# Kernel optimization log

Hardware: AMD Instinct MI355X
Metric: run time of the kernel (lower is better)

## Reference

```python
import jax, jax.numpy as jnp
import numpy as np

BN_EPS = 1e-5

def _vq(x, embed):
    # x: (..., dim), embed: (dim, K). Nearest-codeword lookup with straight-through.
    dim = x.shape[-1]
    flat = x.reshape(-1, dim)
    dist = (flat * flat).sum(1, keepdims=True) - 2.0 * (flat @ embed) + (embed * embed).sum(0, keepdims=True)
    ids = jnp.argmin(dist, axis=1)
    q = jnp.take(embed.T, ids, axis=0).reshape(x.shape)
    diff = jnp.mean((jax.lax.stop_gradient(q) - x) ** 2)
    q = x + jax.lax.stop_gradient(q - x)
    return q, diff

def _weight_quantize(W, embed, in_mem, out_mem):
    # W: (out_f, in_f). Group W.T into (out_g, in_g, in_mem*out_mem) blocks,
    # VQ each block, scatter back to (out_f, in_f). Matches torch chunk/stack loops.
    out_f, in_f = W.shape
    in_g, out_g = in_f // in_mem, out_f // out_mem
    g = W.T.reshape(in_g, in_mem, out_g, out_mem).transpose(2, 0, 1, 3).reshape(out_g, in_g, in_mem * out_mem)
    q, diff = _vq(g, embed)
    qW = q.reshape(out_g, in_g, in_mem, out_mem).transpose(0, 3, 1, 2).reshape(out_f, in_f)
    return qW, diff

def _bn(x, gamma, beta):
    # training-mode BatchNorm1d: biased batch variance
    mu = x.mean(axis=0)
    var = ((x - mu) ** 2).mean(axis=0)
    return (x - mu) * jax.lax.rsqrt(var + BN_EPS) * gamma + beta


def setup_inputs() -> dict:
    key = jax.random.key(0)
    ks = jax.random.split(key, 8)
    B, D_IN, H, D_OUT, K = 65536, 784, 512, 10, 512
    s = 0.05
    return {
        "x": jax.random.normal(ks[0], (B, D_IN), jnp.float32),
        "W1": jax.random.normal(ks[1], (H, D_IN), jnp.float32) * s,
        "b1": jnp.zeros((H,), jnp.float32),
        "gamma1": jnp.ones((H,), jnp.float32),
        "beta1": jnp.zeros((H,), jnp.float32),
        "E1": jax.random.normal(ks[2], (28, K), jnp.float32) * s,  # dim = in_mem(7)*out_mem(4)
        "W2": jax.random.normal(ks[3], (H, H), jnp.float32) * s,
        "b2": jnp.zeros((H,), jnp.float32),
        "E2": jax.random.normal(ks[4], (16, K), jnp.float32) * s,  # dim = in_mem(16)*out_mem(1)
        "W3": jax.random.normal(ks[5], (D_OUT, H), jnp.float32) * s,
        "b3": jnp.zeros((D_OUT,), jnp.float32),
    }


def reference(x, W1, b1, gamma1, beta1, E1, W2, b2, E2, W3, b3):
    qW1, diff1 = _weight_quantize(W1, E1, 7, 4)
    h = jax.nn.relu(x @ qW1.T + b1)
    qW2, diff2 = _weight_quantize(W2, E2, 16, 1)
    h = jax.nn.relu(_bn(h, gamma1, beta1) @ qW2.T + b2)
    out = h @ W3.T + b3
    return out, diff1 + diff2
```

## Files before the change

### kernel.cpp

```cpp
#include <hip/hip_runtime.h>
#include <stdint.h>

#define BATCH   65536
#define D_IN    784
#define KP      800
#define HDIM    512
#define D_OUT   10
#define NCODE   512
#define HT_LD   136

typedef _Float16 f16;
typedef _Float16 f16x8 __attribute__((ext_vector_type(8)));
typedef float    f32x4 __attribute__((ext_vector_type(4)));

__device__ __forceinline__ void gld_lds16(const void* g, void* l) {
  __builtin_amdgcn_global_load_lds((const __attribute__((address_space(1))) void*)g,
                                   (__attribute__((address_space(3))) void*)l, 16, 0, 0);
}

__global__ void k_convert_x(const float* __restrict__ x, f16* __restrict__ xh) {
  int t = blockIdx.x * 256 + threadIdx.x;
  int r = t / 100;
  int c = (t - r * 100) * 8;
  f16x8 o;
  if (c < D_IN) {
    const float4 a = *(const float4*)(x + (size_t)r * D_IN + c);
    const float4 b = *(const float4*)(x + (size_t)r * D_IN + c + 4);
    o[0]=(f16)a.x; o[1]=(f16)a.y; o[2]=(f16)a.z; o[3]=(f16)a.w;
    o[4]=(f16)b.x; o[5]=(f16)b.y; o[6]=(f16)b.z; o[7]=(f16)b.w;
  } else {
    #pragma unroll
    for (int j = 0; j < 8; ++j) o[j] = (f16)0.f;
  }
  *(f16x8*)(xh + (size_t)r * KP + c) = o;
}

__global__ void k_vq1(const float* __restrict__ W1, const float* __restrict__ E1,
                      f16* __restrict__ qW1, float* __restrict__ diffacc) {
  #pragma clang fp contract(off)
  __shared__ float E1s[28 * NCODE];
  __shared__ float Ts[NCODE];
  for (int i = threadIdx.x; i < 28 * NCODE; i += 256) E1s[i] = E1[i];
  __syncthreads();
  for (int k = threadIdx.x; k < NCODE; k += 256) {
    float e0 = E1s[k];
    float t = e0 * e0;
    for (int j = 1; j < 28; ++j) {
      float e = E1s[j * NCODE + k];
      float ee = e * e;
      t = t + ee;
    }
    Ts[k] = t;
  }
  __syncthreads();
  const int wid = threadIdx.x >> 6, lane = threadIdx.x & 63;
  const int bid = blockIdx.x * 4 + wid;
  const int og = bid / 112, ig = bid % 112;
  float v[28], vv[28];
  #pragma unroll
  for (int j = 0; j < 28; ++j) {
    int om = j & 3, im = j >> 2;
    v[j] = W1[(og * 4 + om) * D_IN + ig * 7 + im];
    vv[j] = v[j] * v[j];
  }
  float r[8];
  #pragma unroll
  for (int j = 0; j < 8; ++j) r[j] = vv[j];
  #pragma unroll
  for (int j = 0; j < 8; ++j) r[j] = r[j] + vv[8 + j];
  #pragma unroll
  for (int j = 0; j < 8; ++j) r[j] = r[j] + vv[16 + j];
  float s = ((r[0] + r[1]) + (r[2] + r[3])) + ((r[4] + r[5]) + (r[6] + r[7]));
  s = s + vv[24]; s = s + vv[25]; s = s + vv[26]; s = s + vv[27];

  float bestd = 1e30f; int bestk = 0x7fffffff;
  for (int t = 0; t < 8; ++t) {
    int k = t * 64 + lane;
    float dot = 0.f;
    #pragma unroll
    for (int j = 0; j < 28; ++j) dot = __builtin_fmaf(v[j], E1s[j * NCODE + k], dot);
    float d = (s - 2.0f * dot) + Ts[k];
    if (d < bestd || (d == bestd && k < bestk)) { bestd = d; bestk = k; }
  }
  for (int off = 32; off; off >>= 1) {
    float d2 = __shfl_down(bestd, off, 64);
    int   k2 = __shfl_down(bestk, off, 64);
    if (d2 < bestd || (d2 == bestd && k2 < bestk)) { bestd = d2; bestk = k2; }
  }
  int kstar = __shfl(bestk, 0, 64);
  float sq = 0.f;
  if (lane < 28) {
    int om = lane & 3, im = lane >> 2;
    float q = E1s[lane * NCODE + kstar];
    qW1[(size_t)(og * 4 + om) * KP + ig * 7 + im] = (f16)q;
    float dd = q - v[lane]; sq = dd * dd;
  }
  for (int off = 32; off; off >>= 1) sq += __shfl_down(sq, off, 64);
  if (lane == 0) atomicAdd(&diffacc[bid & 127], sq);
}

__global__ void k_vq2(const float* __restrict__ W2, const float* __restrict__ E2,
                      f16* __restrict__ qW2, float* __restrict__ diffacc) {
  #pragma clang fp contract(off)
  __shared__ float E2s[16 * NCODE];
  __shared__ float Ts[NCODE];
  for (int i = threadIdx.x; i < 16 * NCODE; i += 256) E2s[i] = E2[i];
  __syncthreads();
  for (int k = threadIdx.x; k < NCODE; k += 256) {
    float e0 = E2s[k];
    float t = e0 * e0;
    for (int j = 1; j < 16; ++j) {
      float e = E2s[j * NCODE + k];
      float ee = e * e;
      t = t + ee;
    }
    Ts[k] = t;
  }
  __syncthreads();
  const int wid = threadIdx.x >> 6, lane = threadIdx.x & 63;
  const int bid = blockIdx.x * 4 + wid;
  const int og = bid >> 5, ig = bid & 31;
  float v[16], vv[16];
  #pragma unroll
  for (int j = 0; j < 16; ++j) {
    v[j] = W2[og * HDIM + ig * 16 + j];
    vv[j] = v[j] * v[j];
  }
  float r[8];
  #pragma unroll
  for (int j = 0; j < 8; ++j) r[j] = vv[j];
  #pragma unroll
  for (int j = 0; j < 8; ++j) r[j] = r[j] + vv[8 + j];
  float s = ((r[0] + r[1]) + (r[2] + r[3])) + ((r[4] + r[5]) + (r[6] + r[7]));

  float bestd = 1e30f; int bestk = 0x7fffffff;
  for (int t = 0; t < 8; ++t) {
    int k = t * 64 + lane;
    float dot = 0.f;
    #pragma unroll
    for (int j = 0; j < 16; ++j) dot = __builtin_fmaf(v[j], E2s[j * NCODE + k], dot);
    float d = (s - 2.0f * dot) + Ts[k];
    if (d < bestd || (d == bestd && k < bestk)) { bestd = d; bestk = k; }
  }
  for (int off = 32; off; off >>= 1) {
    float d2 = __shfl_down(bestd, off, 64);
    int   k2 = __shfl_down(bestk, off, 64);
    if (d2 < bestd || (d2 == bestd && k2 < bestk)) { bestd = d2; bestk = k2; }
  }
  int kstar = __shfl(bestk, 0, 64);
  float sq = 0.f;
  if (lane < 16) {
    float q = E2s[lane * NCODE + kstar];
    qW2[(size_t)og * HDIM + ig * 16 + lane] = (f16)q;
    float dd = q - v[lane]; sq = dd * dd;
  }
  for (int off = 32; off; off >>= 1) sq += __shfl_down(sq, off, 64);
  if (lane == 0) atomicAdd(&diffacc[bid & 127], sq);
}

__global__ void k_gemm1(const f16* __restrict__ A, const f16* __restrict__ Bw,
                        const float* __restrict__ bias, f16* __restrict__ C,
                        float* __restrict__ statacc) {
  __shared__ __align__(16) char lds_all[HT_LD * 128 * 2];
  __shared__ float cls[128], cls2[128];
  f16* As = (f16*)lds_all;
  f16* Bs = (f16*)(lds_all + 8192);
  f16* ht = (f16*)lds_all;
  const int tid = threadIdx.x;
  const int bn = blockIdx.x & 3;
  const int bm = blockIdx.x >> 2;
  const int lane = tid & 63, wid = tid >> 6;
  const int waveM = wid & 1, waveN = wid >> 1;
  const int l15 = lane & 15, quad = lane >> 4;

  if (tid < 128) cls[tid] = 0.f; else cls2[tid - 128] = 0.f;

  const int c0 = tid, c1 = tid + 256;
  const f16* gA0 = A + (size_t)(bm * 128 + (c0 >> 2)) * KP + (c0 & 3) * 8;
  const f16* gA1 = A + (size_t)(bm * 128 + (c1 >> 2)) * KP + (c1 & 3) * 8;
  const f16* gB0 = Bw + (size_t)(bn * 128 + (c0 >> 2)) * KP + (c0 & 3) * 8;
  const f16* gB1 = Bw + (size_t)(bn * 128 + (c1 >> 2)) * KP + (c1 & 3) * 8;
  f16* lA0 = As + c0 * 8; f16* lA1 = As + c1 * 8;
  f16* lB0 = Bs + c0 * 8; f16* lB1 = Bs + c1 * 8;

  f32x4 acc[4][4];
  #pragma unroll
  for (int i = 0; i < 4; ++i)
    #pragma unroll
    for (int j = 0; j < 4; ++j) acc[i][j] = (f32x4){0.f, 0.f, 0.f, 0.f};

  const int aoff = (waveM * 64 + l15) * 32 + quad * 8;
  const int boff = (waveN * 64 + l15) * 32 + quad * 8;

  for (int k0 = 0; k0 < KP; k0 += 32) {
    gld_lds16(gA0 + k0, lA0);
    gld_lds16(gA1 + k0, lA1);
    gld_lds16(gB0 + k0, lB0);
    gld_lds16(gB1 + k0, lB1);
    __syncthreads();
    f16x8 af[4], bf[4];
    #pragma unroll
    for (int i = 0; i < 4; ++i) af[i] = *(const f16x8*)(As + aoff + i * 16 * 32);
    #pragma unroll
    for (int j = 0; j < 4; ++j) bf[j] = *(const f16x8*)(Bs + boff + j * 16 * 32);
    #pragma unroll
    for (int i = 0; i < 4; ++i)
      #pragma unroll
      for (int j = 0; j < 4; ++j)
        acc[i][j] = __builtin_amdgcn_mfma_f32_16x16x32_f16(af[i], bf[j], acc[i][j], 0, 0, 0);
    __syncthreads();
  }
  const int colbase = bn * 128 + waveN * 64 + l15;
  float bcol[4];
  #pragma unroll
  for (int j = 0; j < 4; ++j) bcol[j] = bias[colbase + j * 16];
  float cs[4] = {0.f,0.f,0.f,0.f}, cs2[4] = {0.f,0.f,0.f,0.f};
  #pragma unroll
  for (int i = 0; i < 4; ++i)
    #pragma unroll
    for (int r2 = 0; r2 < 4; ++r2) {
      int rloc = waveM * 64 + quad * 4 + i * 16 + r2;
      #pragma unroll
      for (int j = 0; j < 4; ++j) {
        float v = acc[i][j][r2] + bcol[j];
        v = v > 0.f ? v : 0.f;
        ht[rloc * HT_LD + waveN * 64 + j * 16 + l15] = (f16)v;
        cs[j] += v; cs2[j] += v * v;
      }
    }
  #pragma unroll
  for (int j = 0; j < 4; ++j) {
    cs[j]  += __shfl_xor(cs[j], 16, 64);  cs[j]  += __shfl_xor(cs[j], 32, 64);
    cs2[j] += __shfl_xor(cs2[j], 16, 64); cs2[j] += __shfl_xor(cs2[j], 32, 64);
  }
  if (quad == 0) {
    #pragma unroll
    for (int j = 0; j < 4; ++j) {
      atomicAdd(&cls[waveN * 64 + j * 16 + l15], cs[j]);
      atomicAdd(&cls2[waveN * 64 + j * 16 + l15], cs2[j]);
    }
  }
  __syncthreads();
  if (tid < 128) atomicAdd(&statacc[256 + bn * 128 + tid], cls[tid]);
  else           atomicAdd(&statacc[768 + bn * 128 + (tid - 128)], cls2[tid - 128]);
  {
    const int rloc = tid >> 1, half = tid & 1;
    f16* crow = C + (size_t)(bm * 128 + rloc) * HDIM + bn * 128 + half * 64;
    const f16* srow = ht + rloc * HT_LD + half * 64;
    #pragma unroll
    for (int j = 0; j < 8; ++j)
      *(f16x8*)(crow + j * 8) = *(const f16x8*)(srow + j * 8);
  }
}

__global__ void k_bnprep(const float* __restrict__ acc, const float* __restrict__ gamma,
                         const float* __restrict__ beta, float* __restrict__ ab,
                         const float* __restrict__ W3, f16* __restrict__ W3h,
                         float* __restrict__ diff_out) {
  const int c = threadIdx.x;
  const float inv = 1.f / 65536.f;
  float mu = acc[256 + c] * inv;
  float msq = acc[768 + c] * inv;
  float var = msq - mu * mu;
  float a = gamma[c] / sqrtf(var + 1e-5f);
  ab[c] = a;
  ab[512 + c] = beta[c] - mu * a;
  #pragma unroll
  for (int o = 0; o < 16; ++o)
    W3h[o * HDIM + c] = (o < D_OUT) ? (f16)W3[o * HDIM + c] : (f16)0.f;
  if (c == 0) {
    float s1 = 0.f, s2 = 0.f;
    for (int i = 0; i < 128; ++i) { s1 += acc[i]; s2 += acc[128 + i]; }
    diff_out[0] = s1 * (1.f / 401408.f) + s2 * (1.f / 262144.f);
  }
}

__global__ void k_bnfold(f16* __restrict__ qW2, const float* __restrict__ ab,
                         const float* __restrict__ b2, float* __restrict__ bias2) {
  __shared__ float red[256];
  const int n = blockIdx.x, t = threadIdx.x;
  float partial = 0.f;
  #pragma unroll
  for (int kk = 0; kk < 2; ++kk) {
    int k = t + kk * 256;
    float w = (float)qW2[n * HDIM + k];
    partial += ab[512 + k] * w;
    qW2[n * HDIM + k] = (f16)(ab[k] * w);
  }
  red[t] = partial; __syncthreads();
  for (int s = 128; s > 0; s >>= 1) { if (t < s) red[t] += red[t + s]; __syncthreads(); }
  if (t == 0) bias2[n] = b2[n] + red[0];
}

__global__ void k_gemm2f(const f16* __restrict__ A, const f16* __restrict__ Bw,
                         const float* __restrict__ bias2, const f16* __restrict__ W3h,
                         const float* __restrict__ b3, float* __restrict__ out) {
  __shared__ __align__(16) char lds_all[HT_LD * 128 * 2];
  f16* As = (f16*)lds_all;
  f16* Bs = (f16*)(lds_all + 8192);
  f16* ht = (f16*)lds_all;
  const int tid = threadIdx.x;
  const int bn = blockIdx.x & 3;
  const int bm = blockIdx.x >> 2;
  const int lane = tid & 63, wid = tid >> 6;
  const int waveM = wid & 1, waveN = wid >> 1;
  const int l15 = lane & 15, quad = lane >> 4;

  const int c0 = tid, c1 = tid + 256;
  const f16* gA0 = A + (size_t)(bm * 128 + (c0 >> 2)) * HDIM + (c0 & 3) * 8;
  const f16* gA1 = A + (size_t)(bm * 128 + (c1 >> 2)) * HDIM + (c1 & 3) * 8;
  const f16* gB0 = Bw + (size_t)(bn * 128 + (c0 >> 2)) * HDIM + (c0 & 3) * 8;
  const f16* gB1 = Bw + (size_t)(bn * 128 + (c1 >> 2)) * HDIM + (c1 & 3) * 8;
  f16* lA0 = As + c0 * 8; f16* lA1 = As + c1 * 8;
  f16* lB0 = Bs + c0 * 8; f16* lB1 = Bs + c1 * 8;

  f32x4 acc[4][4];
  #pragma unroll
  for (int i = 0; i < 4; ++i)
    #pragma unroll
    for (int j = 0; j < 4; ++j) acc[i][j] = (f32x4){0.f, 0.f, 0.f, 0.f};

  const int aoff = (waveM * 64 + l15) * 32 + quad * 8;
  const int boff = (waveN * 64 + l15) * 32 + quad * 8;

  for (int k0 = 0; k0 < HDIM; k0 += 32) {
    gld_lds16(gA0 + k0, lA0);
    gld_lds16(gA1 + k0, lA1);
    gld_lds16(gB0 + k0, lB0);
    gld_lds16(gB1 + k0, lB1);
    __syncthreads();
    f16x8 af[4], bf[4];
    #pragma unroll
    for (int i = 0; i < 4; ++i) af[i] = *(const f16x8*)(As + aoff + i * 16 * 32);
    #pragma unroll
    for (int j = 0; j < 4; ++j) bf[j] = *(const f16x8*)(Bs + boff + j * 16 * 32);
    #pragma unroll
    for (int i = 0; i < 4; ++i)
      #pragma unroll
      for (int j = 0; j < 4; ++j)
        acc[i][j] = __builtin_amdgcn_mfma_f32_16x16x32_f16(af[i], bf[j], acc[i][j], 0, 0, 0);
    __syncthreads();
  }
  const int colbase = bn * 128 + waveN * 64 + l15;
  float bcol[4];
  #pragma unroll
  for (int j = 0; j < 4; ++j) bcol[j] = bias2[colbase + j * 16];
  #pragma unroll
  for (int i = 0; i < 4; ++i)
    #pragma unroll
    for (int r2 = 0; r2 < 4; ++r2) {
      int rloc = waveM * 64 + quad * 4 + i * 16 + r2;
      #pragma unroll
      for (int j = 0; j < 4; ++j) {
        float v = acc[i][j][r2] + bcol[j];
        v = v > 0.f ? v : 0.f;
        ht[rloc * HT_LD + waveN * 64 + j * 16 + l15] = (f16)v;
      }
    }
  __syncthreads();
  f32x4 oacc[2];
  oacc[0] = (f32x4){0.f,0.f,0.f,0.f}; oacc[1] = (f32x4){0.f,0.f,0.f,0.f};
  #pragma unroll
  for (int ks = 0; ks < 4; ++ks) {
    f16x8 bfr = *(const f16x8*)(W3h + l15 * HDIM + bn * 128 + ks * 32 + quad * 8);
    #pragma unroll
    for (int i2 = 0; i2 < 2; ++i2) {
      f16x8 afr = *(const f16x8*)(ht + (wid * 32 + i2 * 16 + l15) * HT_LD + ks * 32 + quad * 8);
      oacc[i2] = __builtin_amdgcn_mfma_f32_16x16x32_f16(afr, bfr, oacc[i2], 0, 0, 0);
    }
  }
  if (l15 < D_OUT) {
    float badd = (bn == 0) ? b3[l15] : 0.f;
    #pragma unroll
    for (int i2 = 0; i2 < 2; ++i2)
      #pragma unroll
      for (int r2 = 0; r2 < 4; ++r2) {
        int row = bm * 128 + wid * 32 + i2 * 16 + quad * 4 + r2;
        atomicAdd(&out[(size_t)row * D_OUT + l15], oacc[i2][r2] + badd);
      }
  }
}

extern "C" void kernel_launch(void* const* d_in, const int* in_sizes, int n_in,
                              void* d_out, int out_size, void* d_ws, size_t ws_size,
                              hipStream_t stream) {
  const float* x     = (const float*)d_in[0];
  const float* W1    = (const float*)d_in[1];
  const float* b1    = (const float*)d_in[2];
  const float* gamma = (const float*)d_in[3];
  const float* beta  = (const float*)d_in[4];
  const float* E1    = (const float*)d_in[5];
  const float* W2    = (const float*)d_in[6];
  const float* b2    = (const float*)d_in[7];
  const float* E2    = (const float*)d_in[8];
  const float* W3    = (const float*)d_in[9];
  const float* b3    = (const float*)d_in[10];
  float* out = (float*)d_out;

  char* ws = (char*)d_ws;
  float* accum = (float*)ws;
  f16* qW1h = (f16*)(ws + 8192);
  f16* qW2h = (f16*)(ws + 827392);
  f16* W3h  = (f16*)(ws + 1351680);
  float* ab = (float*)(ws + 1368064);
  float* bias2 = (float*)(ws + 1372160);
  f16* xh   = (f16*)(ws + 1376256);
  f16* h    = (f16*)(ws + 106233856);

  hipMemsetAsync(ws, 0, 827392, stream);
  hipMemsetAsync(d_out, 0, (size_t)out_size * 4, stream);
  k_convert_x<<<25600, 256, 0, stream>>>(x, xh);
  k_vq1<<<3584, 256, 0, stream>>>(W1, E1, qW1h, accum);
  k_vq2<<<4096, 256, 0, stream>>>(W2, E2, qW2h, accum + 128);
  k_gemm1<<<2048, 256, 0, stream>>>(xh, qW1h, b1, h, accum);
  k_bnprep<<<1, 512, 0, stream>>>(accum, gamma, beta, ab, W3, W3h, out + (size_t)BATCH * D_OUT);
  k_bnfold<<<512, 256, 0, stream>>>(qW2h, ab, b2, bias2);
  k_gemm2f<<<2048, 256, 0, stream>>>(h, qW2h, bias2, W3h, b3, out);
}
```

Before: 600.5 us.

## Fuse fp32-to-fp16 input conversion into GEMM1 and deepen K tile to 64

```diff
diff --git a/kernel.cpp b/kernel.cpp
--- a/kernel.cpp
+++ b/kernel.cpp
@@ -3,7 +3,7 @@
 
 #define BATCH   65536
 #define D_IN    784
-#define KP      800
+#define KP      832
 #define HDIM    512
 #define D_OUT   10
 #define NCODE   512
@@ -16,23 +16,6 @@
 __device__ __forceinline__ void gld_lds16(const void* g, void* l) {
   __builtin_amdgcn_global_load_lds((const __attribute__((address_space(1))) void*)g,
                                    (__attribute__((address_space(3))) void*)l, 16, 0, 0);
-}
-
-__global__ void k_convert_x(const float* __restrict__ x, f16* __restrict__ xh) {
-  int t = blockIdx.x * 256 + threadIdx.x;
-  int r = t / 100;
-  int c = (t - r * 100) * 8;
-  f16x8 o;
-  if (c < D_IN) {
-    const float4 a = *(const float4*)(x + (size_t)r * D_IN + c);
-    const float4 b = *(const float4*)(x + (size_t)r * D_IN + c + 4);
-    o[0]=(f16)a.x; o[1]=(f16)a.y; o[2]=(f16)a.z; o[3]=(f16)a.w;
-    o[4]=(f16)b.x; o[5]=(f16)b.y; o[6]=(f16)b.z; o[7]=(f16)b.w;
-  } else {
-    #pragma unroll
-    for (int j = 0; j < 8; ++j) o[j] = (f16)0.f;
-  }
-  *(f16x8*)(xh + (size_t)r * KP + c) = o;
 }
 
 __global__ void k_vq1(const float* __restrict__ W1, const float* __restrict__ E1,
@@ -158,30 +141,41 @@
   if (lane == 0) atomicAdd(&diffacc[bid & 127], sq);
 }
 
-__global__ void k_gemm1(const f16* __restrict__ A, const f16* __restrict__ Bw,
-                        const float* __restrict__ bias, f16* __restrict__ C,
-                        float* __restrict__ statacc) {
+__global__ void __launch_bounds__(256, 4)
+k_gemm1(const float* __restrict__ X, const f16* __restrict__ Bw,
+        const float* __restrict__ bias, f16* __restrict__ C,
+        float* __restrict__ statacc) {
   __shared__ __align__(16) char lds_all[HT_LD * 128 * 2];
   __shared__ float cls[128], cls2[128];
   f16* As = (f16*)lds_all;
-  f16* Bs = (f16*)(lds_all + 8192);
+  f16* Bs = (f16*)(lds_all + 16384);
   f16* ht = (f16*)lds_all;
   const int tid = threadIdx.x;
-  const int bn = blockIdx.x & 3;
-  const int bm = blockIdx.x >> 2;
+  const int logical = ((blockIdx.x & 7) << 8) + (blockIdx.x >> 3);
+  const int bn = logical & 3;
+  const int bm = logical >> 2;
   const int lane = tid & 63, wid = tid >> 6;
   const int waveM = wid & 1, waveN = wid >> 1;
   const int l15 = lane & 15, quad = lane >> 4;
 
   if (tid < 128) cls[tid] = 0.f; else cls2[tid - 128] = 0.f;
 
-  const int c0 = tid, c1 = tid + 256;
-  const f16* gA0 = A + (size_t)(bm * 128 + (c0 >> 2)) * KP + (c0 & 3) * 8;
-  const f16* gA1 = A + (size_t)(bm * 128 + (c1 >> 2)) * KP + (c1 & 3) * 8;
-  const f16* gB0 = Bw + (size_t)(bn * 128 + (c0 >> 2)) * KP + (c0 & 3) * 8;
-  const f16* gB1 = Bw + (size_t)(bn * 128 + (c1 >> 2)) * KP + (c1 & 3) * 8;
-  f16* lA0 = As + c0 * 8; f16* lA1 = As + c1 * 8;
-  f16* lB0 = Bs + c0 * 8; f16* lB1 = Bs + c1 * 8;
+  const f16* gB[4]; f16* lB[4];
+  #pragma unroll
+  for (int s = 0; s < 4; ++s) {
+    int slot = tid + s * 256;
+    int ks = slot >> 9, r2 = (slot >> 2) & 127, c = slot & 3;
+    gB[s] = Bw + (size_t)(bn * 128 + r2) * KP + ks * 32 + c * 8;
+    lB[s] = Bs + slot * 8;
+  }
+  const int cA = tid & 3;
+  const float* gA[4]; f16* lA[4];
+  #pragma unroll
+  for (int s = 0; s < 4; ++s) {
+    int r2 = (tid >> 2) + (s & 1) * 64;
+    gA[s] = X + (size_t)(bm * 128 + r2) * D_IN + (s >> 1) * 32 + cA * 8;
+    lA[s] = As + (tid + s * 256) * 8;
+  }
 
   f32x4 acc[4][4];
   #pragma unroll
@@ -192,22 +186,43 @@
   const int aoff = (waveM * 64 + l15) * 32 + quad * 8;
   const int boff = (waveN * 64 + l15) * 32 + quad * 8;
 
-  for (int k0 = 0; k0 < KP; k0 += 32) {
-    gld_lds16(gA0 + k0, lA0);
-    gld_lds16(gA1 + k0, lA1);
-    gld_lds16(gB0 + k0, lB0);
-    gld_lds16(gB1 + k0, lB1);
+  for (int k0 = 0; k0 < KP; k0 += 64) {
+    #pragma unroll
+    for (int s = 0; s < 4; ++s) gld_lds16(gB[s] + k0, lB[s]);
+    float4 ra[8];
+    #pragma unroll
+    for (int s = 0; s < 4; ++s) {
+      int gcol = k0 + (s >> 1) * 32 + cA * 8;
+      ra[2 * s]     = (float4){0.f, 0.f, 0.f, 0.f};
+      ra[2 * s + 1] = (float4){0.f, 0.f, 0.f, 0.f};
+      if (gcol < D_IN) {
+        ra[2 * s]     = *(const float4*)(gA[s] + k0);
+        ra[2 * s + 1] = *(const float4*)(gA[s] + k0 + 4);
+      }
+    }
+    #pragma unroll
+    for (int s = 0; s < 4; ++s) {
+      f16x8 o;
+      o[0] = (f16)ra[2 * s].x;     o[1] = (f16)ra[2 * s].y;
+      o[2] = (f16)ra[2 * s].z;     o[3] = (f16)ra[2 * s].w;
+      o[4] = (f16)ra[2 * s + 1].x; o[5] = (f16)ra[2 * s + 1].y;
+      o[6] = (f16)ra[2 * s + 1].z; o[7] = (f16)ra[2 * s + 1].w;
+      *(f16x8*)lA[s] = o;
+    }
     __syncthreads();
-    f16x8 af[4], bf[4];
-    #pragma unroll
-    for (int i = 0; i < 4; ++i) af[i] = *(const f16x8*)(As + aoff + i * 16 * 32);
-    #pragma unroll
-    for (int j = 0; j < 4; ++j) bf[j] = *(const f16x8*)(Bs + boff + j * 16 * 32);
-    #pragma unroll
-    for (int i = 0; i < 4; ++i)
-      #pragma unroll
-      for (int j = 0; j < 4; ++j)
-        acc[i][j] = __builtin_amdgcn_mfma_f32_16x16x32_f16(af[i], bf[j], acc[i][j], 0, 0, 0);
+    #pragma unroll
+    for (int ks = 0; ks < 2; ++ks) {
+      f16x8 af[4], bf[4];
+      #pragma unroll
+      for (int i = 0; i < 4; ++i) af[i] = *(const f16x8*)(As + ks * 4096 + aoff + i * 512);
+      #pragma unroll
+      for (int j = 0; j < 4; ++j) bf[j] = *(const f16x8*)(Bs + ks * 4096 + boff + j * 512);
+      #pragma unroll
+      for (int i = 0; i < 4; ++i)
+        #pragma unroll
+        for (int j = 0; j < 4; ++j)
+          acc[i][j] = __builtin_amdgcn_mfma_f32_16x16x32_f16(af[i], bf[j], acc[i][j], 0, 0, 0);
+    }
     __syncthreads();
   }
   const int colbase = bn * 128 + waveN * 64 + l15;
@@ -292,27 +307,32 @@
   if (t == 0) bias2[n] = b2[n] + red[0];
 }
 
-__global__ void k_gemm2f(const f16* __restrict__ A, const f16* __restrict__ Bw,
-                         const float* __restrict__ bias2, const f16* __restrict__ W3h,
-                         const float* __restrict__ b3, float* __restrict__ out) {
+__global__ void __launch_bounds__(256, 4)
+k_gemm2f(const f16* __restrict__ A, const f16* __restrict__ Bw,
+         const float* __restrict__ bias2, const f16* __restrict__ W3h,
+         const float* __restrict__ b3, float* __restrict__ out) {
   __shared__ __align__(16) char lds_all[HT_LD * 128 * 2];
   f16* As = (f16*)lds_all;
-  f16* Bs = (f16*)(lds_all + 8192);
+  f16* Bs = (f16*)(lds_all + 16384);
   f16* ht = (f16*)lds_all;
   const int tid = threadIdx.x;
-  const int bn = blockIdx.x & 3;
-  const int bm = blockIdx.x >> 2;
+  const int logical = ((blockIdx.x & 7) << 8) + (blockIdx.x >> 3);
+  const int bn = logical & 3;
+  const int bm = logical >> 2;
   const int lane = tid & 63, wid = tid >> 6;
   const int waveM = wid & 1, waveN = wid >> 1;
   const int l15 = lane & 15, quad = lane >> 4;
 
-  const int c0 = tid, c1 = tid + 256;
-  const f16* gA0 = A + (size_t)(bm * 128 + (c0 >> 2)) * HDIM + (c0 & 3) * 8;
-  const f16* gA1 = A + (size_t)(bm * 128 + (c1 >> 2)) * HDIM + (c1 & 3) * 8;
-  const f16* gB0 = Bw + (size_t)(bn * 128 + (c0 >> 2)) * HDIM + (c0 & 3) * 8;
-  const f16* gB1 = Bw + (size_t)(bn * 128 + (c1 >> 2)) * HDIM + (c1 & 3) * 8;
-  f16* lA0 = As + c0 * 8; f16* lA1 = As + c1 * 8;
-  f16* lB0 = Bs + c0 * 8; f16* lB1 = Bs + c1 * 8;
+  const f16* gA[4]; const f16* gB[4]; f16* lA[4]; f16* lB[4];
+  #pragma unroll
+  for (int s = 0; s < 4; ++s) {
+    int slot = tid + s * 256;
+    int ks = slot >> 9, r2 = (slot >> 2) & 127, c = slot & 3;
+    gA[s] = A  + (size_t)(bm * 128 + r2) * HDIM + ks * 32 + c * 8;
+    gB[s] = Bw + (size_t)(bn * 128 + r2) * HDIM + ks * 32 + c * 8;
+    lA[s] = As + slot * 8;
+    lB[s] = Bs + slot * 8;
+  }
 
   f32x4 acc[4][4];
   #pragma unroll
@@ -323,22 +343,26 @@
   const int aoff = (waveM * 64 + l15) * 32 + quad * 8;
   const int boff = (waveN * 64 + l15) * 32 + quad * 8;
 
-  for (int k0 = 0; k0 < HDIM; k0 += 32) {
-    gld_lds16(gA0 + k0, lA0);
-    gld_lds16(gA1 + k0, lA1);
-    gld_lds16(gB0 + k0, lB0);
-    gld_lds16(gB1 + k0, lB1);
+  for (int k0 = 0; k0 < HDIM; k0 += 64) {
+    #pragma unroll
+    for (int s = 0; s < 4; ++s) {
+      gld_lds16(gA[s] + k0, lA[s]);
+      gld_lds16(gB[s] + k0, lB[s]);
+    }
     __syncthreads();
-    f16x8 af[4], bf[4];
-    #pragma unroll
-    for (int i = 0; i < 4; ++i) af[i] = *(const f16x8*)(As + aoff + i * 16 * 32);
-    #pragma unroll
-    for (int j = 0; j < 4; ++j) bf[j] = *(const f16x8*)(Bs + boff + j * 16 * 32);
-    #pragma unroll
-    for (int i = 0; i < 4; ++i)
-      #pragma unroll
-      for (int j = 0; j < 4; ++j)
-        acc[i][j] = __builtin_amdgcn_mfma_f32_16x16x32_f16(af[i], bf[j], acc[i][j], 0, 0, 0);
+    #pragma unroll
+    for (int ks = 0; ks < 2; ++ks) {
+      f16x8 af[4], bf[4];
+      #pragma unroll
+      for (int i = 0; i < 4; ++i) af[i] = *(const f16x8*)(As + ks * 4096 + aoff + i * 512);
+      #pragma unroll
+      for (int j = 0; j < 4; ++j) bf[j] = *(const f16x8*)(Bs + ks * 4096 + boff + j * 512);
+      #pragma unroll
+      for (int i = 0; i < 4; ++i)
+        #pragma unroll
+        for (int j = 0; j < 4; ++j)
+          acc[i][j] = __builtin_amdgcn_mfma_f32_16x16x32_f16(af[i], bf[j], acc[i][j], 0, 0, 0);
+    }
     __syncthreads();
   }
   const int colbase = bn * 128 + waveN * 64 + l15;
@@ -400,19 +424,17 @@
   char* ws = (char*)d_ws;
   float* accum = (float*)ws;
   f16* qW1h = (f16*)(ws + 8192);
-  f16* qW2h = (f16*)(ws + 827392);
-  f16* W3h  = (f16*)(ws + 1351680);
-  float* ab = (float*)(ws + 1368064);
-  float* bias2 = (float*)(ws + 1372160);
-  f16* xh   = (f16*)(ws + 1376256);
-  f16* h    = (f16*)(ws + 106233856);
-
-  hipMemsetAsync(ws, 0, 827392, stream);
+  f16* qW2h = (f16*)(ws + 860160);
+  f16* W3h  = (f16*)(ws + 1384448);
+  float* ab = (float*)(ws + 1400832);
+  float* bias2 = (float*)(ws + 1404928);
+  f16* h    = (f16*)(ws + 1409024);
+
+  hipMemsetAsync(ws, 0, 860160, stream);
   hipMemsetAsync(d_out, 0, (size_t)out_size * 4, stream);
-  k_convert_x<<<25600, 256, 0, stream>>>(x, xh);
   k_vq1<<<3584, 256, 0, stream>>>(W1, E1, qW1h, accum);
   k_vq2<<<4096, 256, 0, stream>>>(W2, E2, qW2h, accum + 128);
-  k_gemm1<<<2048, 256, 0, stream>>>(xh, qW1h, b1, h, accum);
+  k_gemm1<<<2048, 256, 0, stream>>>(x, qW1h, b1, h, accum);
   k_bnprep<<<1, 512, 0, stream>>>(accum, gamma, beta, ab, W3, W3h, out + (size_t)BATCH * D_OUT);
   k_bnfold<<<512, 256, 0, stream>>>(qW2h, ab, b2, bias2);
   k_gemm2f<<<2048, 256, 0, stream>>>(h, qW2h, bias2, W3h, b3, out);
```

After: 564.1 us. -6.1%, faster.

## Fuse fp32-to-fp16 x conversion into GEMM1 and double-buffer both GEMM main loops

Applied to the files above, without the earlier changes.

```diff
diff --git a/kernel.cpp b/kernel.cpp
--- a/kernel.cpp
+++ b/kernel.cpp
@@ -18,22 +18,8 @@
                                    (__attribute__((address_space(3))) void*)l, 16, 0, 0);
 }
 
-__global__ void k_convert_x(const float* __restrict__ x, f16* __restrict__ xh) {
-  int t = blockIdx.x * 256 + threadIdx.x;
-  int r = t / 100;
-  int c = (t - r * 100) * 8;
-  f16x8 o;
-  if (c < D_IN) {
-    const float4 a = *(const float4*)(x + (size_t)r * D_IN + c);
-    const float4 b = *(const float4*)(x + (size_t)r * D_IN + c + 4);
-    o[0]=(f16)a.x; o[1]=(f16)a.y; o[2]=(f16)a.z; o[3]=(f16)a.w;
-    o[4]=(f16)b.x; o[5]=(f16)b.y; o[6]=(f16)b.z; o[7]=(f16)b.w;
-  } else {
-    #pragma unroll
-    for (int j = 0; j < 8; ++j) o[j] = (f16)0.f;
-  }
-  *(f16x8*)(xh + (size_t)r * KP + c) = o;
-}
+#define MEMFENCE asm volatile("" ::: "memory")
+#define BARRIER() do { MEMFENCE; __builtin_amdgcn_s_barrier(); MEMFENCE; } while (0)
 
 __global__ void k_vq1(const float* __restrict__ W1, const float* __restrict__ E1,
                       f16* __restrict__ qW1, float* __restrict__ diffacc) {
@@ -158,30 +144,29 @@
   if (lane == 0) atomicAdd(&diffacc[bid & 127], sq);
 }
 
-__global__ void k_gemm1(const f16* __restrict__ A, const f16* __restrict__ Bw,
-                        const float* __restrict__ bias, f16* __restrict__ C,
-                        float* __restrict__ statacc) {
+__global__ void __launch_bounds__(256, 4)
+k_gemm1(const float* __restrict__ X, const f16* __restrict__ Bw,
+        const float* __restrict__ bias, f16* __restrict__ C,
+        float* __restrict__ statacc) {
   __shared__ __align__(16) char lds_all[HT_LD * 128 * 2];
   __shared__ float cls[128], cls2[128];
-  f16* As = (f16*)lds_all;
-  f16* Bs = (f16*)(lds_all + 8192);
   f16* ht = (f16*)lds_all;
   const int tid = threadIdx.x;
-  const int bn = blockIdx.x & 3;
-  const int bm = blockIdx.x >> 2;
+  const int logical = ((blockIdx.x & 7) << 8) + (blockIdx.x >> 3);
+  const int bn = logical & 3;
+  const int bm = logical >> 2;
   const int lane = tid & 63, wid = tid >> 6;
   const int waveM = wid & 1, waveN = wid >> 1;
   const int l15 = lane & 15, quad = lane >> 4;
 
   if (tid < 128) cls[tid] = 0.f; else cls2[tid - 128] = 0.f;
 
-  const int c0 = tid, c1 = tid + 256;
-  const f16* gA0 = A + (size_t)(bm * 128 + (c0 >> 2)) * KP + (c0 & 3) * 8;
-  const f16* gA1 = A + (size_t)(bm * 128 + (c1 >> 2)) * KP + (c1 & 3) * 8;
-  const f16* gB0 = Bw + (size_t)(bn * 128 + (c0 >> 2)) * KP + (c0 & 3) * 8;
-  const f16* gB1 = Bw + (size_t)(bn * 128 + (c1 >> 2)) * KP + (c1 & 3) * 8;
-  f16* lA0 = As + c0 * 8; f16* lA1 = As + c1 * 8;
-  f16* lB0 = Bs + c0 * 8; f16* lB1 = Bs + c1 * 8;
+  const int cA = tid & 3;
+  const int r0 = tid >> 2;
+  const float* gX0 = X + (size_t)(bm * 128 + r0) * D_IN;
+  const float* gX1 = gX0 + (size_t)64 * D_IN;
+  const f16*  gB0 = Bw + (size_t)(bn * 128 + r0) * KP + cA * 8;
+  const f16*  gB1 = gB0 + (size_t)64 * KP;
 
   f32x4 acc[4][4];
   #pragma unroll
@@ -192,23 +177,77 @@
   const int aoff = (waveM * 64 + l15) * 32 + quad * 8;
   const int boff = (waveN * 64 + l15) * 32 + quad * 8;
 
-  for (int k0 = 0; k0 < KP; k0 += 32) {
-    gld_lds16(gA0 + k0, lA0);
-    gld_lds16(gA1 + k0, lA1);
-    gld_lds16(gB0 + k0, lB0);
-    gld_lds16(gB1 + k0, lB1);
-    __syncthreads();
+  float4 ra0, ra1, ra2, ra3;
+  auto issueA = [&](int k0) {
+    int gc = k0 + cA * 8;
+    int gco = gc < D_IN ? gc : 0;
+    ra0 = *(const float4*)(gX0 + gco);
+    ra1 = *(const float4*)(gX0 + gco + 4);
+    ra2 = *(const float4*)(gX1 + gco);
+    ra3 = *(const float4*)(gX1 + gco + 4);
+  };
+  auto writeA = [&](int k0, f16* dstA) {
+    bool valid = (k0 + cA * 8) < D_IN;
+    float4 a0 = ra0, a1 = ra1, b0 = ra2, b1 = ra3;
+    if (!valid) {
+      a0 = (float4){0.f,0.f,0.f,0.f}; a1 = a0; b0 = a0; b1 = a0;
+    }
+    f16x8 o0, o1;
+    o0[0]=(f16)a0.x; o0[1]=(f16)a0.y; o0[2]=(f16)a0.z; o0[3]=(f16)a0.w;
+    o0[4]=(f16)a1.x; o0[5]=(f16)a1.y; o0[6]=(f16)a1.z; o0[7]=(f16)a1.w;
+    o1[0]=(f16)b0.x; o1[1]=(f16)b0.y; o1[2]=(f16)b0.z; o1[3]=(f16)b0.w;
+    o1[4]=(f16)b1.x; o1[5]=(f16)b1.y; o1[6]=(f16)b1.z; o1[7]=(f16)b1.w;
+    *(f16x8*)(dstA + tid * 8) = o0;
+    *(f16x8*)(dstA + tid * 8 + 2048) = o1;
+  };
+  auto issueB = [&](int k0, f16* dstB) {
+    gld_lds16(gB0 + k0, dstB + tid * 8);
+    gld_lds16(gB1 + k0, dstB + tid * 8 + 2048);
+  };
+  auto mma = [&](const f16* A_, const f16* B_) {
     f16x8 af[4], bf[4];
     #pragma unroll
-    for (int i = 0; i < 4; ++i) af[i] = *(const f16x8*)(As + aoff + i * 16 * 32);
-    #pragma unroll
-    for (int j = 0; j < 4; ++j) bf[j] = *(const f16x8*)(Bs + boff + j * 16 * 32);
+    for (int i = 0; i < 4; ++i) af[i] = *(const f16x8*)(A_ + aoff + i * 512);
+    #pragma unroll
+    for (int j = 0; j < 4; ++j) bf[j] = *(const f16x8*)(B_ + boff + j * 512);
     #pragma unroll
     for (int i = 0; i < 4; ++i)
       #pragma unroll
       for (int j = 0; j < 4; ++j)
         acc[i][j] = __builtin_amdgcn_mfma_f32_16x16x32_f16(af[i], bf[j], acc[i][j], 0, 0, 0);
-    __syncthreads();
+  };
+
+  const int NT = KP / 32;
+  issueA(0);
+  MEMFENCE;
+  issueB(0, (f16*)(lds_all + 16384));
+  MEMFENCE;
+  writeA(0, (f16*)lds_all);
+  issueA(32);
+  asm volatile("s_waitcnt vmcnt(4) lgkmcnt(0)" ::: "memory");
+  BARRIER();
+
+  for (int k = 0; k < NT; ++k) {
+    const int cur = k & 1;
+    f16* Asc = (f16*)(lds_all + cur * 8192);
+    f16* Bsc = (f16*)(lds_all + 16384 + cur * 8192);
+    f16* Asn = (f16*)(lds_all + (cur ^ 1) * 8192);
+    f16* Bsn = (f16*)(lds_all + 16384 + (cur ^ 1) * 8192);
+    if (k + 1 < NT) issueB((k + 1) * 32, Bsn);
+    MEMFENCE;
+    __builtin_amdgcn_s_setprio(1);
+    mma(Asc, Bsc);
+    __builtin_amdgcn_s_setprio(0);
+    if (k + 1 < NT) {
+      writeA((k + 1) * 32, Asn);
+      if (k + 2 < NT) {
+        issueA((k + 2) * 32);
+        asm volatile("s_waitcnt vmcnt(4) lgkmcnt(0)" ::: "memory");
+      } else {
+        asm volatile("s_waitcnt vmcnt(0) lgkmcnt(0)" ::: "memory");
+      }
+    }
+    BARRIER();
   }
   const int colbase = bn * 128 + waveN * 64 + l15;
   float bcol[4];
@@ -292,27 +331,24 @@
   if (t == 0) bias2[n] = b2[n] + red[0];
 }
 
-__global__ void k_gemm2f(const f16* __restrict__ A, const f16* __restrict__ Bw,
-                         const float* __restrict__ bias2, const f16* __restrict__ W3h,
-                         const float* __restrict__ b3, float* __restrict__ out) {
+__global__ void __launch_bounds__(256, 4)
+k_gemm2f(const f16* __restrict__ A, const f16* __restrict__ Bw,
+         const float* __restrict__ bias2, const f16* __restrict__ W3h,
+         const float* __restrict__ b3, float* __restrict__ out) {
   __shared__ __align__(16) char lds_all[HT_LD * 128 * 2];
-  f16* As = (f16*)lds_all;
-  f16* Bs = (f16*)(lds_all + 8192);
   f16* ht = (f16*)lds_all;
   const int tid = threadIdx.x;
-  const int bn = blockIdx.x & 3;
-  const int bm = blockIdx.x >> 2;
+  const int logical = ((blockIdx.x & 7) << 8) + (blockIdx.x >> 3);
+  const int bn = logical & 3;
+  const int bm = logical >> 2;
   const int lane = tid & 63, wid = tid >> 6;
   const int waveM = wid & 1, waveN = wid >> 1;
   const int l15 = lane & 15, quad = lane >> 4;
 
-  const int c0 = tid, c1 = tid + 256;
-  const f16* gA0 = A + (size_t)(bm * 128 + (c0 >> 2)) * HDIM + (c0 & 3) * 8;
-  const f16* gA1 = A + (size_t)(bm * 128 + (c1 >> 2)) * HDIM + (c1 & 3) * 8;
-  const f16* gB0 = Bw + (size_t)(bn * 128 + (c0 >> 2)) * HDIM + (c0 & 3) * 8;
-  const f16* gB1 = Bw + (size_t)(bn * 128 + (c1 >> 2)) * HDIM + (c1 & 3) * 8;
-  f16* lA0 = As + c0 * 8; f16* lA1 = As + c1 * 8;
-  f16* lB0 = Bs + c0 * 8; f16* lB1 = Bs + c1 * 8;
+  const f16* gA0 = A  + (size_t)(bm * 128 + (tid >> 2)) * HDIM + (tid & 3) * 8;
+  const f16* gA1 = gA0 + (size_t)64 * HDIM;
+  const f16* gB0 = Bw + (size_t)(bn * 128 + (tid >> 2)) * HDIM + (tid & 3) * 8;
+  const f16* gB1 = gB0 + (size_t)64 * HDIM;
 
   f32x4 acc[4][4];
   #pragma unroll
@@ -323,23 +359,41 @@
   const int aoff = (waveM * 64 + l15) * 32 + quad * 8;
   const int boff = (waveN * 64 + l15) * 32 + quad * 8;
 
-  for (int k0 = 0; k0 < HDIM; k0 += 32) {
-    gld_lds16(gA0 + k0, lA0);
-    gld_lds16(gA1 + k0, lA1);
-    gld_lds16(gB0 + k0, lB0);
-    gld_lds16(gB1 + k0, lB1);
-    __syncthreads();
+  auto issueT = [&](int k0, int b) {
+    f16* As_ = (f16*)(lds_all + b * 8192);
+    f16* Bs_ = (f16*)(lds_all + 16384 + b * 8192);
+    gld_lds16(gA0 + k0, As_ + tid * 8);
+    gld_lds16(gA1 + k0, As_ + tid * 8 + 2048);
+    gld_lds16(gB0 + k0, Bs_ + tid * 8);
+    gld_lds16(gB1 + k0, Bs_ + tid * 8 + 2048);
+  };
+  auto mma = [&](const f16* A_, const f16* B_) {
     f16x8 af[4], bf[4];
     #pragma unroll
-    for (int i = 0; i < 4; ++i) af[i] = *(const f16x8*)(As + aoff + i * 16 * 32);
-    #pragma unroll
-    for (int j = 0; j < 4; ++j) bf[j] = *(const f16x8*)(Bs + boff + j * 16 * 32);
+    for (int i = 0; i < 4; ++i) af[i] = *(const f16x8*)(A_ + aoff + i * 512);
+    #pragma unroll
+    for (int j = 0; j < 4; ++j) bf[j] = *(const f16x8*)(B_ + boff + j * 512);
     #pragma unroll
     for (int i = 0; i < 4; ++i)
       #pragma unroll
       for (int j = 0; j < 4; ++j)
         acc[i][j] = __builtin_amdgcn_mfma_f32_16x16x32_f16(af[i], bf[j], acc[i][j], 0, 0, 0);
-    __syncthreads();
+  };
+
+  const int NT = HDIM / 32;
+  issueT(0, 0);
+  asm volatile("s_waitcnt vmcnt(0)" ::: "memory");
+  BARRIER();
+
+  for (int k = 0; k < NT; ++k) {
+    const int cur = k & 1;
+    if (k + 1 < NT) issueT((k + 1) * 32, cur ^ 1);
+    MEMFENCE;
+    __builtin_amdgcn_s_setprio(1);
+    mma((f16*)(lds_all + cur * 8192), (f16*)(lds_all + 16384 + cur * 8192));
+    __builtin_amdgcn_s_setprio(0);
+    if (k + 1 < NT) asm volatile("s_waitcnt vmcnt(0)" ::: "memory");
+    BARRIER();
   }
   const int colbase = bn * 128 + waveN * 64 + l15;
   float bcol[4];
@@ -404,15 +458,13 @@
   f16* W3h  = (f16*)(ws + 1351680);
   float* ab = (float*)(ws + 1368064);
   float* bias2 = (float*)(ws + 1372160);
-  f16* xh   = (f16*)(ws + 1376256);
-  f16* h    = (f16*)(ws + 106233856);
+  f16* h    = (f16*)(ws + 1376256);
 
   hipMemsetAsync(ws, 0, 827392, stream);
   hipMemsetAsync(d_out, 0, (size_t)out_size * 4, stream);
-  k_convert_x<<<25600, 256, 0, stream>>>(x, xh);
   k_vq1<<<3584, 256, 0, stream>>>(W1, E1, qW1h, accum);
   k_vq2<<<4096, 256, 0, stream>>>(W2, E2, qW2h, accum + 128);
-  k_gemm1<<<2048, 256, 0, stream>>>(xh, qW1h, b1, h, accum);
+  k_gemm1<<<2048, 256, 0, stream>>>(x, qW1h, b1, h, accum);
   k_bnprep<<<1, 512, 0, stream>>>(accum, gamma, beta, ab, W3, W3h, out + (size_t)BATCH * D_OUT);
   k_bnfold<<<512, 256, 0, stream>>>(qW2h, ab, b2, bias2);
   k_gemm2f<<<2048, 256, 0, stream>>>(h, qW2h, bias2, W3h, b3, out);
```

After: 545.9 us. 1.1x faster.
